# Kernel optimization log

Hardware: AMD Instinct MI355X
Metric: run time of the kernel (lower is better)

The kernel has to match this reference:

```python
import jax, jax.numpy as jnp
import numpy as np

V_TH = 1.0  # spikingjelly IFNode default threshold; v starts at 0, hard reset after fire


def setup_inputs() -> dict:
    key = jax.random.key(0)
    k_x, k_w1, k_w2 = jax.random.split(key, 3)
    B, IN, FEAT, OUT = 4096, 3136, 6272, 500
    # binary input spikes (LatencyEncoder emits 0/1 spikes per timestep)
    x = (jax.random.uniform(k_x, (B, IN)) < 0.5).astype(jnp.float32)
    # Linear weights, torch layout [out_features, in_features], kaiming-ish scale
    W1 = jax.random.normal(k_w1, (FEAT, IN), dtype=jnp.float32) / np.sqrt(IN)
    W2 = jax.random.normal(k_w2, (OUT, FEAT), dtype=jnp.float32) / np.sqrt(FEAT)
    return {"x": x, "W1": W1, "W2": W2}


def reference(x, W1, W2):
    # Linear (no bias) -> IF neuron single step: v = 0 + I; spike = (v >= V_TH); hard reset
    v1 = x @ W1.T                      # [B, FEAT]
    s1 = (v1 >= V_TH).astype(x.dtype)  # binary hidden spikes
    v2 = s1 @ W2.T                     # [B, OUT]
    s2 = (v2 >= V_TH).astype(x.dtype)  # output spikes
    return s2
```

## Files before the change

kernel.cpp:

```cpp
#include <hip/hip_runtime.h>


namespace {
constexpr int kB = 4096;
constexpr int kIn = 3136;
constexpr int kFeat = 6272;
constexpr int kFeatWords = 196;
constexpr int kOut = 500;
constexpr size_t kPlane1 = (size_t)kFeat * kIn;
constexpr size_t kW1F = 3 * kPlane1;
constexpr size_t kW2F = (size_t)784 * 12288;
constexpr size_t kS1Bytes = (size_t)kB * kFeatWords * 4;
constexpr size_t kXb2Bytes = (size_t)49 * kB * 8;
constexpr unsigned kCap1 = 2u << 20;
constexpr unsigned kCap2 = 1u << 16;
__device__ constexpr double kTau1 = 7.4769e-4;
__device__ constexpr double kTau2 = 1.4955e-3;
}

typedef int v4i __attribute__((ext_vector_type(4)));
typedef int v16i __attribute__((ext_vector_type(16)));

__device__ __forceinline__ void gload_lds16(const void* g, void* l) {
  __builtin_amdgcn_global_load_lds((__attribute__((address_space(1))) void*)(g),
                                   (__attribute__((address_space(3))) void*)(l),
                                   16, 0, 0);
}

__device__ __forceinline__ v4i expand16(unsigned b) {
  unsigned u0 = (((b      ) & 0xFu) * 0x204081u) & 0x01010101u;
  unsigned u1 = (((b >> 4 ) & 0xFu) * 0x204081u) & 0x01010101u;
  unsigned u2 = (((b >> 8 ) & 0xFu) * 0x204081u) & 0x01010101u;
  unsigned u3 = (((b >> 12) & 0xFu) * 0x204081u) & 0x01010101u;
  return (v4i){(int)u0, (int)u1, (int)u2, (int)u3};
}

__device__ __forceinline__ void split3(float w, signed char* d) {
  float c = rintf(w * 128.f);
  d[0] = (signed char)(int)c;
  float r = fmaf(c, -7.8125e-03f, w);
  c = rintf(r * 16384.f);
  d[1] = (signed char)(int)c;
  r = fmaf(c, -6.103515625e-05f, r);
  c = rintf(r * 2097152.f);
  d[2] = (signed char)(int)c;
}

__global__ __launch_bounds__(256) void conv_w1F(const float* __restrict__ W,
                                                signed char* __restrict__ F) {
  const int bx = blockIdx.x;
  const int fb = bx / 49;
  const int kt = bx % 49;
  const int f = threadIdx.x & 63;
  const int g = threadIdx.x >> 6;
  const float* src = W + (size_t)(fb * 64 + f) * kIn + kt * 64 + g * 16;
  union { signed char c[16]; int4 v; } o[3];
#pragma unroll
  for (int q = 0; q < 4; ++q) {
    const float4 w = *(const float4*)(src + q * 4);
    signed char d[4][3];
    split3(w.x, d[0]); split3(w.y, d[1]); split3(w.z, d[2]); split3(w.w, d[3]);
#pragma unroll
    for (int e = 0; e < 4; ++e)
#pragma unroll
      for (int j = 0; j < 3; ++j) o[j].c[q * 4 + e] = d[e][j];
  }
#pragma unroll
  for (int j = 0; j < 3; ++j)
    *(int4*)(F + ((size_t)bx * 3 + j) * 4096 + g * 1024 + f * 16) = o[j].v;
}

__global__ __launch_bounds__(256) void conv_w2F(const float* __restrict__ W,
                                                signed char* __restrict__ F) {
  const int bx = blockIdx.x;
  const int fb = bx / 98;
  const int kt = bx % 98;
  const int f = threadIdx.x & 63;
  const int g = threadIdx.x >> 6;
  const int feat = fb * 64 + f;
  union { signed char c[16]; int4 v; } o[3];
#pragma unroll
  for (int q = 0; q < 4; ++q) {
    float4 w = {0.f, 0.f, 0.f, 0.f};
    if (feat < kOut)
      w = *(const float4*)(W + (size_t)feat * kFeat + kt * 64 + g * 16 + q * 4);
    signed char d[4][3];
    split3(w.x, d[0]); split3(w.y, d[1]); split3(w.z, d[2]); split3(w.w, d[3]);
#pragma unroll
    for (int e = 0; e < 4; ++e)
#pragma unroll
      for (int j = 0; j < 3; ++j) o[j].c[q * 4 + e] = d[e][j];
  }
#pragma unroll
  for (int j = 0; j < 3; ++j)
    *(int4*)(F + ((size_t)bx * 3 + j) * 4096 + g * 1024 + f * 16) = o[j].v;
}

__global__ __launch_bounds__(256) void pack_x2(const float* __restrict__ X,
                                               uint2* __restrict__ xb2) {
  const int wid = (blockIdx.x * 256 + threadIdx.x) >> 6;
  const int lane = threadIdx.x & 63;
  const int b = wid / 49;
  const int g = wid % 49;
  const float v = X[(size_t)b * kIn + g * 64 + lane];
  const unsigned long long bal = __ballot(v != 0.f);
  if (lane == 0) xb2[(size_t)g * kB + b] = make_uint2((unsigned)bal, (unsigned)(bal >> 32));
}

__global__ __launch_bounds__(512, 2) void fc1_v4(
    const uint2* __restrict__ xb2, const signed char* __restrict__ w1lF,
    unsigned* __restrict__ s1b, unsigned* __restrict__ s1T,
    unsigned* __restrict__ cnt, unsigned* __restrict__ list) {
  __shared__ __align__(16) signed char lds[24576];
  const int tid = threadIdx.x;
  const int lane = tid & 63;
  const int ln31 = lane & 31;
  const int half = lane >> 5;
  const int wv = tid >> 6;
  const int waveM = wv >> 1;
  const int waveN = wv & 1;
  const int bx = blockIdx.y;
  const int bM = blockIdx.x * 256;

  const signed char* const gbase = w1lF + (size_t)bx * 49 * 12288;
  const bool has1 = (wv < 4);
  const unsigned sG0 = wv * 1024u + lane * 16u;
  const unsigned sL0 = wv * 1024u;
  const unsigned sG1 = (wv + 8) * 1024u + lane * 16u;
  const unsigned sL1 = (wv + 8) * 1024u;

  const uint2* const aptr = xb2 + bM + waveM * 64 + ln31;
  const unsigned bfeat = (waveN * 32 + ln31) * 16u;

  v16i acc[2][3] = {};
  uint2 abC[2], abN[2];
#pragma unroll
  for (int m = 0; m < 2; ++m) abC[m] = aptr[m * 32];
  gload_lds16(gbase + sG0, lds + sL0);
  if (has1) gload_lds16(gbase + sG1, lds + sL1);

  for (int kt = 0; kt < 49; ++kt) {
    __syncthreads();
    const int cb = (kt & 1) * 12288;
    if (kt < 48) {
      const int nb = ((kt + 1) & 1) * 12288;
      const size_t go = (size_t)(kt + 1) * 12288;
      gload_lds16(gbase + go + sG0, lds + nb + sL0);
      if (has1) gload_lds16(gbase + go + sG1, lds + nb + sL1);
#pragma unroll
      for (int m = 0; m < 2; ++m) abN[m] = aptr[(size_t)(kt + 1) * kB + m * 32];
    }
#pragma unroll
    for (int kk = 0; kk < 2; ++kk) {
      const unsigned gsel = (kk * 2 + half) * 1024u;
      const v4i b0 = *(const v4i*)(lds + cb + 0 * 4096 + gsel + bfeat);
      const v4i b1 = *(const v4i*)(lds + cb + 1 * 4096 + gsel + bfeat);
      const v4i b2 = *(const v4i*)(lds + cb + 2 * 4096 + gsel + bfeat);
#pragma unroll
      for (int m = 0; m < 2; ++m) {
        const unsigned word = kk ? abC[m].y : abC[m].x;
        const v4i a = expand16((word >> (half * 16)) & 0xFFFFu);
        acc[m][0] = __builtin_amdgcn_mfma_i32_32x32x32_i8(a, b0, acc[m][0], 0, 0, 0);
        acc[m][1] = __builtin_amdgcn_mfma_i32_32x32x32_i8(a, b1, acc[m][1], 0, 0, 0);
        acc[m][2] = __builtin_amdgcn_mfma_i32_32x32x32_i8(a, b2, acc[m][2], 0, 0, 0);
      }
    }
    abC[0] = abN[0];
    abC[1] = abN[1];
  }

  const double s7 = 0.0078125;
  const int word = bx * 2 + waveN;
  const int fcol = word * 32 + ln31;
#pragma unroll
  for (int m = 0; m < 2; ++m) {
#pragma unroll
    for (int t = 0; t < 16; ++t) {
      double v = (double)acc[m][2][t];
      v = v * s7 + (double)acc[m][1][t];
      v = v * s7 + (double)acc[m][0][t];
      v = v * s7;
      const unsigned long long bal = __ballot(v >= 1.0);
      const int mrow = bM + waveM * 64 + m * 32 + (t & 3) + 8 * (t >> 2);
      if (lane == 0) {
        s1b[(size_t)mrow * kFeatWords + word] = (unsigned)bal;
        s1T[(size_t)word * kB + mrow] = (unsigned)bal;
      }
      if (lane == 32) {
        s1b[(size_t)(mrow + 4) * kFeatWords + word] = (unsigned)(bal >> 32);
        s1T[(size_t)word * kB + mrow + 4] = (unsigned)(bal >> 32);
      }
      if (fabs(v - 1.0) <= kTau1) {
        const unsigned idx = atomicAdd(cnt, 1u);
        if (idx < kCap1) list[idx] = ((unsigned)(mrow + 4 * half) << 13) | (unsigned)fcol;
      }
    }
  }
}

__global__ __launch_bounds__(256) void fc1_correct(
    const float* __restrict__ x, const float* __restrict__ W1,
    const unsigned* __restrict__ cnt, const unsigned* __restrict__ list,
    unsigned* __restrict__ s1b, unsigned* __restrict__ s1T) {
  const unsigned n = min(cnt[0], kCap1);
  const int lane = threadIdx.x & 63;
  const int wid = (blockIdx.x * 256 + threadIdx.x) >> 6;
  const int nw = (gridDim.x * 256) >> 6;
  for (unsigned i = wid; i < n; i += nw) {
    const unsigned u = list[i];
    const int b = (int)(u >> 13);
    const int f = (int)(u & 8191u);
    double s = 0.0;
    for (int k = lane; k < kIn; k += 64)
      s = fma((double)x[(size_t)b * kIn + k], (double)W1[(size_t)f * kIn + k], s);
#pragma unroll
    for (int off = 32; off > 0; off >>= 1) s += __shfl_down(s, off);
    if (lane == 0) {
      const unsigned mask = 1u << (f & 31);
      unsigned* p1 = s1b + (size_t)b * kFeatWords + (f >> 5);
      unsigned* p2 = s1T + (size_t)(f >> 5) * kB + b;
      if (s >= 1.0) { atomicOr(p1, mask); atomicOr(p2, mask); }
      else          { atomicAnd(p1, ~mask); atomicAnd(p2, ~mask); }
    }
  }
}

__global__ __launch_bounds__(512, 2) void fc2_v4(
    const unsigned* __restrict__ s1T, const signed char* __restrict__ w2lF,
    float* __restrict__ out, unsigned* __restrict__ cnt,
    unsigned* __restrict__ list) {
  __shared__ __align__(16) signed char lds[24576];
  const int tid = threadIdx.x;
  const int lane = tid & 63;
  const int ln31 = lane & 31;
  const int half = lane >> 5;
  const int wv = tid >> 6;
  const int waveM = wv >> 1;
  const int waveN = wv & 1;
  const int bx = blockIdx.y;
  const int bM = blockIdx.x * 128;

  const signed char* const gbase = w2lF + (size_t)bx * 98 * 12288;
  const bool has1 = (wv < 4);
  const unsigned sG0 = wv * 1024u + lane * 16u;
  const unsigned sL0 = wv * 1024u;
  const unsigned sG1 = (wv + 8) * 1024u + lane * 16u;
  const unsigned sL1 = (wv + 8) * 1024u;

  const unsigned* const aptr = s1T + bM + waveM * 32 + ln31;
  const unsigned bfeat = (waveN * 32 + ln31) * 16u;

  v16i acc[3] = {};
  unsigned abC[2], abN[2];
#pragma unroll
  for (int kk = 0; kk < 2; ++kk) abC[kk] = aptr[(size_t)kk * kB];
  gload_lds16(gbase + sG0, lds + sL0);
  if (has1) gload_lds16(gbase + sG1, lds + sL1);

  for (int kt = 0; kt < 98; ++kt) {
    __syncthreads();
    const int cb = (kt & 1) * 12288;
    if (kt < 97) {
      const int nb = ((kt + 1) & 1) * 12288;
      const size_t go = (size_t)(kt + 1) * 12288;
      gload_lds16(gbase + go + sG0, lds + nb + sL0);
      if (has1) gload_lds16(gbase + go + sG1, lds + nb + sL1);
#pragma unroll
      for (int kk = 0; kk < 2; ++kk)
        abN[kk] = aptr[((size_t)(kt + 1) * 2 + kk) * kB];
    }
#pragma unroll
    for (int kk = 0; kk < 2; ++kk) {
      const unsigned gsel = (kk * 2 + half) * 1024u;
      const v4i b0 = *(const v4i*)(lds + cb + 0 * 4096 + gsel + bfeat);
      const v4i b1 = *(const v4i*)(lds + cb + 1 * 4096 + gsel + bfeat);
      const v4i b2 = *(const v4i*)(lds + cb + 2 * 4096 + gsel + bfeat);
      const v4i a = expand16((abC[kk] >> (half * 16)) & 0xFFFFu);
      acc[0] = __builtin_amdgcn_mfma_i32_32x32x32_i8(a, b0, acc[0], 0, 0, 0);
      acc[1] = __builtin_amdgcn_mfma_i32_32x32x32_i8(a, b1, acc[1], 0, 0, 0);
      acc[2] = __builtin_amdgcn_mfma_i32_32x32x32_i8(a, b2, acc[2], 0, 0, 0);
    }
    abC[0] = abN[0];
    abC[1] = abN[1];
  }

  const double s7 = 0.0078125;
  const int o = bx * 64 + waveN * 32 + ln31;
#pragma unroll
  for (int t = 0; t < 16; ++t) {
    double v = (double)acc[2][t];
    v = v * s7 + (double)acc[1][t];
    v = v * s7 + (double)acc[0][t];
    v = v * s7;
    const int b = bM + waveM * 32 + (t & 3) + 8 * (t >> 2) + 4 * half;
    if (o < kOut) {
      out[(size_t)b * kOut + o] = (v >= 1.0) ? 1.0f : 0.0f;
      if (fabs(v - 1.0) <= kTau2) {
        const unsigned idx = atomicAdd(cnt, 1u);
        if (idx < kCap2) list[idx] = ((unsigned)b << 13) | (unsigned)o;
      }
    }
  }
}

__global__ __launch_bounds__(256) void fc2_correct(
    const unsigned* __restrict__ s1b, const float* __restrict__ W2,
    const unsigned* __restrict__ cnt, const unsigned* __restrict__ list,
    float* __restrict__ out) {
  const unsigned n = min(cnt[0], kCap2);
  const int lane = threadIdx.x & 63;
  const int wid = (blockIdx.x * 256 + threadIdx.x) >> 6;
  const int nw = (gridDim.x * 256) >> 6;
  for (unsigned i = wid; i < n; i += nw) {
    const unsigned u = list[i];
    const int b = (int)(u >> 13);
    const int o = (int)(u & 8191u);
    double s = 0.0;
    for (int k = lane; k < kFeat; k += 64) {
      const unsigned w = s1b[(size_t)b * kFeatWords + (k >> 5)];
      if ((w >> (k & 31)) & 1u) s += (double)W2[(size_t)o * kFeat + k];
    }
#pragma unroll
    for (int off = 32; off > 0; off >>= 1) s += __shfl_down(s, off);
    if (lane == 0) out[(size_t)b * kOut + o] = (s >= 1.0) ? 1.0f : 0.0f;
  }
}

__global__ __launch_bounds__(256) void snn_fc1(const float* __restrict__ x,
                                               const float* __restrict__ W1,
                                               unsigned int* __restrict__ s1bits) {
  __shared__ double Xd[32][66];
  __shared__ double Wd[32][66];
  __shared__ unsigned int spikes[64][2];
  const int tid = threadIdx.x;
  const int tx = tid & 15;
  const int ty = tid >> 4;
  const int b0 = blockIdx.y * 64;
  const int f0 = blockIdx.x * 64;
  if (tid < 128) spikes[tid >> 1][tid & 1] = 0u;
  double acc[4][4];
#pragma unroll
  for (int j = 0; j < 4; ++j)
#pragma unroll
    for (int i = 0; i < 4; ++i) acc[j][i] = 0.0;
  const int rl = tid >> 2;
  const int kq = (tid & 3) * 8;
  const float* xrow = x + (size_t)(b0 + rl) * kIn + kq;
  const float* wrow = W1 + (size_t)(f0 + rl) * kIn + kq;
  for (int kc = 0; kc < kIn; kc += 32) {
    const float4 xv0 = *(const float4*)(xrow + kc);
    const float4 xv1 = *(const float4*)(xrow + kc + 4);
    const float4 wv0 = *(const float4*)(wrow + kc);
    const float4 wv1 = *(const float4*)(wrow + kc + 4);
    __syncthreads();
    Xd[kq + 0][rl] = (double)xv0.x; Xd[kq + 1][rl] = (double)xv0.y;
    Xd[kq + 2][rl] = (double)xv0.z; Xd[kq + 3][rl] = (double)xv0.w;
    Xd[kq + 4][rl] = (double)xv1.x; Xd[kq + 5][rl] = (double)xv1.y;
    Xd[kq + 6][rl] = (double)xv1.z; Xd[kq + 7][rl] = (double)xv1.w;
    Wd[kq + 0][rl] = (double)wv0.x; Wd[kq + 1][rl] = (double)wv0.y;
    Wd[kq + 2][rl] = (double)wv0.z; Wd[kq + 3][rl] = (double)wv0.w;
    Wd[kq + 4][rl] = (double)wv1.x; Wd[kq + 5][rl] = (double)wv1.y;
    Wd[kq + 6][rl] = (double)wv1.z; Wd[kq + 7][rl] = (double)wv1.w;
    __syncthreads();
#pragma unroll
    for (int k = 0; k < 32; ++k) {
      const double2 xa = *(const double2*)&Xd[k][ty * 4];
      const double2 xb = *(const double2*)&Xd[k][ty * 4 + 2];
      const double2 wa = *(const double2*)&Wd[k][tx * 4];
      const double2 wb = *(const double2*)&Wd[k][tx * 4 + 2];
      const double xv[4] = {xa.x, xa.y, xb.x, xb.y};
      const double wv[4] = {wa.x, wa.y, wb.x, wb.y};
#pragma unroll
      for (int j = 0; j < 4; ++j)
#pragma unroll
        for (int i = 0; i < 4; ++i) acc[j][i] += xv[j] * wv[i];
    }
  }
  __syncthreads();
#pragma unroll
  for (int j = 0; j < 4; ++j) {
    unsigned int nib = 0u;
#pragma unroll
    for (int i = 0; i < 4; ++i) nib |= (acc[j][i] >= 1.0 ? 1u : 0u) << i;
    atomicOr(&spikes[ty * 4 + j][tx >> 3], nib << ((tx * 4) & 31));
  }
  __syncthreads();
  if (tid < 128) {
    const int r = tid >> 1;
    const int w = tid & 1;
    s1bits[(size_t)(b0 + r) * kFeatWords + (f0 >> 5) + w] = spikes[r][w];
  }
}

__global__ __launch_bounds__(256) void snn_fc2(const unsigned int* __restrict__ s1bits,
                                               const float* __restrict__ W2,
                                               float* __restrict__ out) {
  __shared__ double Wd[32][66];
  __shared__ unsigned int Sb[64];
  const int tid = threadIdx.x;
  const int tx = tid & 15;
  const int ty = tid >> 4;
  const int b0 = blockIdx.y * 64;
  const int o0 = blockIdx.x * 64;
  double acc[4][4];
#pragma unroll
  for (int j = 0; j < 4; ++j)
#pragma unroll
    for (int i = 0; i < 4; ++i) acc[j][i] = 0.0;
  const int rl = tid >> 2;
  const int kq = (tid & 3) * 8;
  int orow = o0 + rl;
  if (orow >= kOut) orow = kOut - 1;
  const float* wrow = W2 + (size_t)orow * kFeat + kq;
  for (int kc = 0; kc < kFeat; kc += 32) {
    const float4 wv0 = *(const float4*)(wrow + kc);
    const float4 wv1 = *(const float4*)(wrow + kc + 4);
    unsigned int sword = 0u;
    if (tid < 64) sword = s1bits[(size_t)(b0 + tid) * kFeatWords + (kc >> 5)];
    __syncthreads();
    Wd[kq + 0][rl] = (double)wv0.x; Wd[kq + 1][rl] = (double)wv0.y;
    Wd[kq + 2][rl] = (double)wv0.z; Wd[kq + 3][rl] = (double)wv0.w;
    Wd[kq + 4][rl] = (double)wv1.x; Wd[kq + 5][rl] = (double)wv1.y;
    Wd[kq + 6][rl] = (double)wv1.z; Wd[kq + 7][rl] = (double)wv1.w;
    if (tid < 64) Sb[tid] = sword;
    __syncthreads();
    const unsigned int rw0 = Sb[ty * 4 + 0];
    const unsigned int rw1 = Sb[ty * 4 + 1];
    const unsigned int rw2 = Sb[ty * 4 + 2];
    const unsigned int rw3 = Sb[ty * 4 + 3];
#pragma unroll
    for (int k = 0; k < 32; ++k) {
      const double2 wa = *(const double2*)&Wd[k][tx * 4];
      const double2 wb = *(const double2*)&Wd[k][tx * 4 + 2];
      const double wv[4] = {wa.x, wa.y, wb.x, wb.y};
      const double sv[4] = {(double)((rw0 >> k) & 1u), (double)((rw1 >> k) & 1u),
                            (double)((rw2 >> k) & 1u), (double)((rw3 >> k) & 1u)};
#pragma unroll
      for (int j = 0; j < 4; ++j)
#pragma unroll
        for (int i = 0; i < 4; ++i) acc[j][i] += sv[j] * wv[i];
    }
  }
#pragma unroll
  for (int j = 0; j < 4; ++j) {
    const int b = b0 + ty * 4 + j;
#pragma unroll
    for (int i = 0; i < 4; ++i) {
      const int o = o0 + tx * 4 + i;
      if (o < kOut) out[(size_t)b * kOut + o] = (acc[j][i] >= 1.0) ? 1.0f : 0.0f;
    }
  }
}

extern "C" void kernel_launch(void* const* d_in, const int* in_sizes, int n_in,
                              void* d_out, int out_size, void* d_ws, size_t ws_size,
                              hipStream_t stream) {
  const float* x = (const float*)d_in[0];
  const float* W1 = (const float*)d_in[1];
  const float* W2 = (const float*)d_in[2];
  float* out = (float*)d_out;

  char* p = (char*)d_ws;
  signed char* w1lF = (signed char*)p;   p += kW1F;
  signed char* w2lF = (signed char*)p;   p += kW2F;
  unsigned* s1b = (unsigned*)p;          p += kS1Bytes;
  unsigned* s1T = (unsigned*)p;          p += kS1Bytes;
  uint2* xb2 = (uint2*)p;                p += kXb2Bytes;
  unsigned* list1 = (unsigned*)p;        p += (size_t)kCap1 * 4;
  unsigned* list2 = (unsigned*)p;        p += (size_t)kCap2 * 4;
  unsigned* ctrs = (unsigned*)p;         p += 256;
  const size_t need = (size_t)(p - (char*)d_ws);

  if (ws_size >= need) {
    hipMemsetAsync(ctrs, 0, 32, stream);
    conv_w1F<<<4802, 256, 0, stream>>>(W1, w1lF);
    conv_w2F<<<784, 256, 0, stream>>>(W2, w2lF);
    pack_x2<<<50176, 256, 0, stream>>>(x, xb2);
    fc1_v4<<<dim3(16, 98), 512, 0, stream>>>(xb2, w1lF, s1b, s1T, ctrs, list1);
    fc1_correct<<<1024, 256, 0, stream>>>(x, W1, ctrs, list1, s1b, s1T);
    fc2_v4<<<dim3(32, 8), 512, 0, stream>>>(s1T, w2lF, out, ctrs + 4, list2);
    fc2_correct<<<64, 256, 0, stream>>>(s1b, W2, ctrs + 4, list2, out);
  } else {
    unsigned* s1 = (unsigned*)d_ws;
    snn_fc1<<<dim3(98, 64), 256, 0, stream>>>(x, W1, s1);
    snn_fc2<<<dim3(8, 64), 256, 0, stream>>>(s1, W2, out);
  }
}
```

Measured before the change: 654.5 us.

## Replace LDS-staged weight tiles with direct register double-buffered global loads

Both GEMM kernels drop the shared-memory double buffer and the per-tile __syncthreads. Each lane now loads its weight fragments straight from global memory into registers, with two register sets alternating across K tiles. Blocks shrink to 256 threads with 64-row M tiles, and fc1 keeps one M fragment per wave instead of two. This removes barrier and LDS traffic and raises occupancy, but weights are no longer shared across waves through LDS, so each wave reads them from global memory or cache separately, multiplying weight traffic.

```diff
diff --git a/kernel.cpp b/kernel.cpp
--- a/kernel.cpp
+++ b/kernel.cpp
@@ -21,12 +21,6 @@
 typedef int v4i __attribute__((ext_vector_type(4)));
 typedef int v16i __attribute__((ext_vector_type(16)));
 
-__device__ __forceinline__ void gload_lds16(const void* g, void* l) {
-  __builtin_amdgcn_global_load_lds((__attribute__((address_space(1))) void*)(g),
-                                   (__attribute__((address_space(3))) void*)(l),
-                                   16, 0, 0);
-}
-
 __device__ __forceinline__ v4i expand16(unsigned b) {
   unsigned u0 = (((b      ) & 0xFu) * 0x204081u) & 0x01010101u;
   unsigned u1 = (((b >> 4 ) & 0xFu) * 0x204081u) & 0x01010101u;
@@ -107,11 +101,10 @@
   if (lane == 0) xb2[(size_t)g * kB + b] = make_uint2((unsigned)bal, (unsigned)(bal >> 32));
 }
 
-__global__ __launch_bounds__(512, 2) void fc1_v4(
+__global__ __launch_bounds__(256, 4) void fc1_v5(
     const uint2* __restrict__ xb2, const signed char* __restrict__ w1lF,
     unsigned* __restrict__ s1b, unsigned* __restrict__ s1T,
     unsigned* __restrict__ cnt, unsigned* __restrict__ list) {
-  __shared__ __align__(16) signed char lds[24576];
   const int tid = threadIdx.x;
   const int lane = tid & 63;
   const int ln31 = lane & 31;
@@ -120,82 +113,77 @@
   const int waveM = wv >> 1;
   const int waveN = wv & 1;
   const int bx = blockIdx.y;
-  const int bM = blockIdx.x * 256;
-
-  const signed char* const gbase = w1lF + (size_t)bx * 49 * 12288;
-  const bool has1 = (wv < 4);
-  const unsigned sG0 = wv * 1024u + lane * 16u;
-  const unsigned sL0 = wv * 1024u;
-  const unsigned sG1 = (wv + 8) * 1024u + lane * 16u;
-  const unsigned sL1 = (wv + 8) * 1024u;
-
-  const uint2* const aptr = xb2 + bM + waveM * 64 + ln31;
-  const unsigned bfeat = (waveN * 32 + ln31) * 16u;
-
-  v16i acc[2][3] = {};
-  uint2 abC[2], abN[2];
-#pragma unroll
-  for (int m = 0; m < 2; ++m) abC[m] = aptr[m * 32];
-  gload_lds16(gbase + sG0, lds + sL0);
-  if (has1) gload_lds16(gbase + sG1, lds + sL1);
-
-  for (int kt = 0; kt < 49; ++kt) {
-    __syncthreads();
-    const int cb = (kt & 1) * 12288;
-    if (kt < 48) {
-      const int nb = ((kt + 1) & 1) * 12288;
-      const size_t go = (size_t)(kt + 1) * 12288;
-      gload_lds16(gbase + go + sG0, lds + nb + sL0);
-      if (has1) gload_lds16(gbase + go + sG1, lds + nb + sL1);
-#pragma unroll
-      for (int m = 0; m < 2; ++m) abN[m] = aptr[(size_t)(kt + 1) * kB + m * 32];
-    }
-#pragma unroll
-    for (int kk = 0; kk < 2; ++kk) {
-      const unsigned gsel = (kk * 2 + half) * 1024u;
-      const v4i b0 = *(const v4i*)(lds + cb + 0 * 4096 + gsel + bfeat);
-      const v4i b1 = *(const v4i*)(lds + cb + 1 * 4096 + gsel + bfeat);
-      const v4i b2 = *(const v4i*)(lds + cb + 2 * 4096 + gsel + bfeat);
-#pragma unroll
-      for (int m = 0; m < 2; ++m) {
-        const unsigned word = kk ? abC[m].y : abC[m].x;
-        const v4i a = expand16((word >> (half * 16)) & 0xFFFFu);
-        acc[m][0] = __builtin_amdgcn_mfma_i32_32x32x32_i8(a, b0, acc[m][0], 0, 0, 0);
-        acc[m][1] = __builtin_amdgcn_mfma_i32_32x32x32_i8(a, b1, acc[m][1], 0, 0, 0);
-        acc[m][2] = __builtin_amdgcn_mfma_i32_32x32x32_i8(a, b2, acc[m][2], 0, 0, 0);
-      }
-    }
-    abC[0] = abN[0];
-    abC[1] = abN[1];
-  }
+  const int bM = blockIdx.x * 64;
+
+  const int row = bM + waveM * 32 + ln31;
+  const uint2* const aptr = xb2 + row;
+  const int fl = waveN * 32 + ln31;
+  const signed char* const bbase =
+      w1lF + (size_t)(bx * 49) * 12288 + half * 1024u + fl * 16u;
+
+  v16i acc[3] = {};
+  v4i b0[6], b1[6];
+  uint2 a0, a1;
+
+#define LOAD_TILE(nk, bf, ab)                                   \
+  {                                                             \
+    const signed char* bp = bbase + (size_t)(nk) * 12288;       \
+    bf[0] = *(const v4i*)(bp);                                  \
+    bf[1] = *(const v4i*)(bp + 2048);                           \
+    bf[2] = *(const v4i*)(bp + 4096);                           \
+    bf[3] = *(const v4i*)(bp + 6144);                           \
+    bf[4] = *(const v4i*)(bp + 8192);                           \
+    bf[5] = *(const v4i*)(bp + 10240);                          \
+    ab = aptr[(size_t)(nk) * kB];                               \
+  }
+#define COMPUTE_TILE(bf, ab)                                                    \
+  {                                                                             \
+    _Pragma("unroll")                                                           \
+    for (int kk = 0; kk < 2; ++kk) {                                            \
+      const unsigned word = kk ? (ab).y : (ab).x;                               \
+      const v4i a = expand16((word >> (half * 16)) & 0xFFFFu);                  \
+      acc[0] = __builtin_amdgcn_mfma_i32_32x32x32_i8(a, bf[kk], acc[0], 0,0,0); \
+      acc[1] = __builtin_amdgcn_mfma_i32_32x32x32_i8(a, bf[2+kk], acc[1],0,0,0);\
+      acc[2] = __builtin_amdgcn_mfma_i32_32x32x32_i8(a, bf[4+kk], acc[2],0,0,0);\
+    }                                                                           \
+  }
+
+  LOAD_TILE(0, b0, a0);
+  for (int kt = 0; kt + 2 <= 49; kt += 2) {
+    LOAD_TILE(kt + 1, b1, a1);
+    COMPUTE_TILE(b0, a0);
+    const int nk2 = (kt + 2 < 49) ? kt + 2 : 48;
+    LOAD_TILE(nk2, b0, a0);
+    COMPUTE_TILE(b1, a1);
+  }
+  COMPUTE_TILE(b0, a0);
 
   const double s7 = 0.0078125;
   const int word = bx * 2 + waveN;
   const int fcol = word * 32 + ln31;
 #pragma unroll
-  for (int m = 0; m < 2; ++m) {
-#pragma unroll
-    for (int t = 0; t < 16; ++t) {
-      double v = (double)acc[m][2][t];
-      v = v * s7 + (double)acc[m][1][t];
-      v = v * s7 + (double)acc[m][0][t];
-      v = v * s7;
-      const unsigned long long bal = __ballot(v >= 1.0);
-      const int mrow = bM + waveM * 64 + m * 32 + (t & 3) + 8 * (t >> 2);
-      if (lane == 0) {
-        s1b[(size_t)mrow * kFeatWords + word] = (unsigned)bal;
-        s1T[(size_t)word * kB + mrow] = (unsigned)bal;
-      }
-      if (lane == 32) {
-        s1b[(size_t)(mrow + 4) * kFeatWords + word] = (unsigned)(bal >> 32);
-        s1T[(size_t)word * kB + mrow + 4] = (unsigned)(bal >> 32);
-      }
-      if (fabs(v - 1.0) <= kTau1) {
-        const unsigned idx = atomicAdd(cnt, 1u);
-        if (idx < kCap1) list[idx] = ((unsigned)(mrow + 4 * half) << 13) | (unsigned)fcol;
-      }
-    }
-  }
+  for (int t = 0; t < 16; ++t) {
+    double v = (double)acc[2][t];
+    v = v * s7 + (double)acc[1][t];
+    v = v * s7 + (double)acc[0][t];
+    v = v * s7;
+    const unsigned long long bal = __ballot(v >= 1.0);
+    const int mrow = bM + waveM * 32 + (t & 3) + 8 * (t >> 2);
+    if (lane == 0) {
+      s1b[(size_t)mrow * kFeatWords + word] = (unsigned)bal;
+      s1T[(size_t)word * kB + mrow] = (unsigned)bal;
+    }
+    if (lane == 32) {
+      s1b[(size_t)(mrow + 4) * kFeatWords + word] = (unsigned)(bal >> 32);
+      s1T[(size_t)word * kB + mrow + 4] = (unsigned)(bal >> 32);
+    }
+    if (fabs(v - 1.0) <= kTau1) {
+      const unsigned idx = atomicAdd(cnt, 1u);
+      if (idx < kCap1) list[idx] = ((unsigned)(mrow + 4 * half) << 13) | (unsigned)fcol;
+    }
+  }
+#undef LOAD_TILE
+#undef COMPUTE_TILE
 }
 
 __global__ __launch_bounds__(256) void fc1_correct(
@@ -225,11 +213,10 @@
   }
 }
 
-__global__ __launch_bounds__(512, 2) void fc2_v4(
+__global__ __launch_bounds__(256, 4) void fc2_v5(
     const unsigned* __restrict__ s1T, const signed char* __restrict__ w2lF,
     float* __restrict__ out, unsigned* __restrict__ cnt,
     unsigned* __restrict__ list) {
-  __shared__ __align__(16) signed char lds[24576];
   const int tid = threadIdx.x;
   const int lane = tid & 63;
   const int ln31 = lane & 31;
@@ -238,50 +225,49 @@
   const int waveM = wv >> 1;
   const int waveN = wv & 1;
   const int bx = blockIdx.y;
-  const int bM = blockIdx.x * 128;
-
-  const signed char* const gbase = w2lF + (size_t)bx * 98 * 12288;
-  const bool has1 = (wv < 4);
-  const unsigned sG0 = wv * 1024u + lane * 16u;
-  const unsigned sL0 = wv * 1024u;
-  const unsigned sG1 = (wv + 8) * 1024u + lane * 16u;
-  const unsigned sL1 = (wv + 8) * 1024u;
-
-  const unsigned* const aptr = s1T + bM + waveM * 32 + ln31;
-  const unsigned bfeat = (waveN * 32 + ln31) * 16u;
+  const int bM = blockIdx.x * 64;
+
+  const int row = bM + waveM * 32 + ln31;
+  const unsigned* const aptr = s1T + row;
+  const int fl = waveN * 32 + ln31;
+  const signed char* const bbase =
+      w2lF + (size_t)(bx * 98) * 12288 + half * 1024u + fl * 16u;
 
   v16i acc[3] = {};
-  unsigned abC[2], abN[2];
-#pragma unroll
-  for (int kk = 0; kk < 2; ++kk) abC[kk] = aptr[(size_t)kk * kB];
-  gload_lds16(gbase + sG0, lds + sL0);
-  if (has1) gload_lds16(gbase + sG1, lds + sL1);
-
-  for (int kt = 0; kt < 98; ++kt) {
-    __syncthreads();
-    const int cb = (kt & 1) * 12288;
-    if (kt < 97) {
-      const int nb = ((kt + 1) & 1) * 12288;
-      const size_t go = (size_t)(kt + 1) * 12288;
-      gload_lds16(gbase + go + sG0, lds + nb + sL0);
-      if (has1) gload_lds16(gbase + go + sG1, lds + nb + sL1);
-#pragma unroll
-      for (int kk = 0; kk < 2; ++kk)
-        abN[kk] = aptr[((size_t)(kt + 1) * 2 + kk) * kB];
-    }
-#pragma unroll
-    for (int kk = 0; kk < 2; ++kk) {
-      const unsigned gsel = (kk * 2 + half) * 1024u;
-      const v4i b0 = *(const v4i*)(lds + cb + 0 * 4096 + gsel + bfeat);
-      const v4i b1 = *(const v4i*)(lds + cb + 1 * 4096 + gsel + bfeat);
-      const v4i b2 = *(const v4i*)(lds + cb + 2 * 4096 + gsel + bfeat);
-      const v4i a = expand16((abC[kk] >> (half * 16)) & 0xFFFFu);
-      acc[0] = __builtin_amdgcn_mfma_i32_32x32x32_i8(a, b0, acc[0], 0, 0, 0);
-      acc[1] = __builtin_amdgcn_mfma_i32_32x32x32_i8(a, b1, acc[1], 0, 0, 0);
-      acc[2] = __builtin_amdgcn_mfma_i32_32x32x32_i8(a, b2, acc[2], 0, 0, 0);
-    }
-    abC[0] = abN[0];
-    abC[1] = abN[1];
+  v4i b0[6], b1[6];
+  uint2 a0, a1;
+
+#define LOAD_TILE(nk, bf, ab)                                   \
+  {                                                             \
+    const signed char* bp = bbase + (size_t)(nk) * 12288;       \
+    bf[0] = *(const v4i*)(bp);                                  \
+    bf[1] = *(const v4i*)(bp + 2048);                           \
+    bf[2] = *(const v4i*)(bp + 4096);                           \
+    bf[3] = *(const v4i*)(bp + 6144);                           \
+    bf[4] = *(const v4i*)(bp + 8192);                           \
+    bf[5] = *(const v4i*)(bp + 10240);                          \
+    (ab).x = aptr[(size_t)((nk) * 2) * kB];                     \
+    (ab).y = aptr[(size_t)((nk) * 2 + 1) * kB];                 \
+  }
+#define COMPUTE_TILE(bf, ab)                                                    \
+  {                                                                             \
+    _Pragma("unroll")                                                           \
+    for (int kk = 0; kk < 2; ++kk) {                                            \
+      const unsigned word = kk ? (ab).y : (ab).x;                               \
+      const v4i a = expand16((word >> (half * 16)) & 0xFFFFu);                  \
+      acc[0] = __builtin_amdgcn_mfma_i32_32x32x32_i8(a, bf[kk], acc[0], 0,0,0); \
+      acc[1] = __builtin_amdgcn_mfma_i32_32x32x32_i8(a, bf[2+kk], acc[1],0,0,0);\
+      acc[2] = __builtin_amdgcn_mfma_i32_32x32x32_i8(a, bf[4+kk], acc[2],0,0,0);\
+    }                                                                           \
+  }
+
+  LOAD_TILE(0, b0, a0);
+  for (int kt = 0; kt + 2 <= 98; kt += 2) {
+    LOAD_TILE(kt + 1, b1, a1);
+    COMPUTE_TILE(b0, a0);
+    const int nk2 = (kt + 2 < 98) ? kt + 2 : 97;
+    LOAD_TILE(nk2, b0, a0);
+    COMPUTE_TILE(b1, a1);
   }
 
   const double s7 = 0.0078125;
@@ -301,6 +287,8 @@
       }
     }
   }
+#undef LOAD_TILE
+#undef COMPUTE_TILE
 }
 
 __global__ __launch_bounds__(256) void fc2_correct(
@@ -476,9 +464,9 @@
     conv_w1F<<<4802, 256, 0, stream>>>(W1, w1lF);
     conv_w2F<<<784, 256, 0, stream>>>(W2, w2lF);
     pack_x2<<<50176, 256, 0, stream>>>(x, xb2);
-    fc1_v4<<<dim3(16, 98), 512, 0, stream>>>(xb2, w1lF, s1b, s1T, ctrs, list1);
+    fc1_v5<<<dim3(64, 98), 256, 0, stream>>>(xb2, w1lF, s1b, s1T, ctrs, list1);
     fc1_correct<<<1024, 256, 0, stream>>>(x, W1, ctrs, list1, s1b, s1T);
-    fc2_v4<<<dim3(32, 8), 512, 0, stream>>>(s1T, w2lF, out, ctrs + 4, list2);
+    fc2_v5<<<dim3(64, 8), 256, 0, stream>>>(s1T, w2lF, out, ctrs + 4, list2);
     fc2_correct<<<64, 256, 0, stream>>>(s1b, W2, ctrs + 4, list2, out);
   } else {
     unsigned* s1 = (unsigned*)d_ws;
```

Result: faster. 630.2 us (-3.7%).
